# Kernel tuning notes

Hardware: AMD Instinct MI355X
Metric: run time of the kernel (lower is better)

## Reference

```python
import jax, jax.numpy as jnp
import numpy as np

B, S, H = 8, 512, 1024          # batch, seq_len, hidden_size
T, K, FF = 8, 2, 4096           # num_thoughts, top_k, ffn dim (4*H)
NH = 8                          # combiner attention heads
HD = H // NH
CREATIVITY = 1.0


def setup_inputs() -> dict:
    key = jax.random.key(0)
    ks = jax.random.split(key, 16)
    s = 0.02
    return {
        "hidden_states": jax.random.normal(ks[0], (B, S, H), jnp.float32),
        # router
        "router_w": jax.random.normal(ks[1], (H, T), jnp.float32) * s,
        "router_b": jnp.zeros((T,), jnp.float32),
        # thought branch FFNs (one per thought)
        "W1": jax.random.normal(ks[2], (T, H, FF), jnp.float32) * s,
        "b1": jnp.zeros((T, FF), jnp.float32),
        "W2": jax.random.normal(ks[3], (T, FF, H), jnp.float32) * s,
        "b2": jnp.zeros((T, H), jnp.float32),
        # attention combiner (MultiheadAttention proj weights)
        "Wq": jax.random.normal(ks[4], (H, H), jnp.float32) * s,
        "bq": jnp.zeros((H,), jnp.float32),
        "Wk": jax.random.normal(ks[5], (H, H), jnp.float32) * s,
        "bk": jnp.zeros((H,), jnp.float32),
        "Wv": jax.random.normal(ks[6], (H, H), jnp.float32) * s,
        "bv": jnp.zeros((H,), jnp.float32),
        "Wo": jax.random.normal(ks[7], (H, H), jnp.float32) * s,
        "bo": jnp.zeros((H,), jnp.float32),
    }


def reference(hidden_states, router_w, router_b, W1, b1, W2, b2,
              Wq, bq, Wk, bk, Wv, bv, Wo, bo):
    # ---- router: mean-pool -> linear -> softmax -> top-k ----
    pooled = hidden_states.mean(axis=1)                       # [B,H]
    router_probs = jax.nn.softmax(pooled @ router_w + router_b, axis=-1)  # [B,T]
    top_p, top_i = jax.lax.top_k(router_probs, K)             # [B,K]
    weights = jax.nn.softmax(top_p, axis=-1)                  # renormalized active weights [B,K]

    # ---- grouped branch FFN (gather expert weights, batched GEMMs) ----
    h = jnp.einsum('bsh,bkhf->bksf', hidden_states, W1[top_i]) + b1[top_i][:, :, None, :]
    h = jax.nn.gelu(h, approximate=False)
    branch_out = jnp.einsum('bksf,bkfh->bksh', h, W2[top_i]) + b2[top_i][:, :, None, :]
    branch_out = branch_out * CREATIVITY                      # [B,K,S,H]

    # ---- attention combiner over flattened thoughts [B, K*S, H] ----
    L = K * S
    flat = branch_out.reshape(B, L, H)
    q = (flat @ Wq + bq).reshape(B, L, NH, HD)
    k = (flat @ Wk + bk).reshape(B, L, NH, HD)
    v = (flat @ Wv + bv).reshape(B, L, NH, HD)
    scores = jnp.einsum('blhd,bmhd->bhlm', q, k) / jnp.sqrt(jnp.float32(HD))
    attn = jax.nn.softmax(scores, axis=-1)
    ctx = jnp.einsum('bhlm,bmhd->blhd', attn, v).reshape(B, L, H)
    attended = (ctx @ Wo + bo).reshape(B, K, S, H)

    combined = jnp.einsum('bksh,bk->bsh', attended, weights)  # [B,S,H]

    # ---- metrics ----
    entropy = jnp.mean(-jnp.sum(router_probs * jnp.log(router_probs + 1e-8), axis=1))
    a = branch_out[:, 0].reshape(B, -1)
    b_ = branch_out[:, 1].reshape(B, -1)
    cos = jnp.sum(a * b_, -1) / jnp.maximum(
        jnp.linalg.norm(a, axis=-1) * jnp.linalg.norm(b_, axis=-1), 1e-8)
    diversity = jnp.mean(1.0 - cos)
    return combined, entropy, diversity
```

## Files before the change

### kernel.cpp

```cpp
#include <hip/hip_runtime.h>
#include <hip/hip_bf16.h>
#include <math.h>

typedef float f32x4 __attribute__((ext_vector_type(4)));
typedef short s16x8 __attribute__((ext_vector_type(8)));
typedef short s16x4 __attribute__((ext_vector_type(4)));
typedef unsigned int u32;

#define DEVI __device__ __forceinline__

#define Bn   8
#define Sn   512
#define Hn   1024
#define Tn   8
#define Kn   2
#define FFn  4096
#define NHn  8
#define HDn  128
#define Ln   1024
#define OUT_COMBINED 4194304

DEVI unsigned short f2bf(float x) {
  __hip_bfloat16 h = __float2bfloat16(x);
  union { __hip_bfloat16 h; unsigned short u; } cv; cv.h = h; return cv.u;
}
DEVI float bf2f(unsigned short u) {
  union { u32 i; float f; } cv; cv.i = ((u32)u) << 16; return cv.f;
}
DEVI float gelu_f(float x) {
  float t = x * x * x;
  float y = 0.7978845608028654f * x + 0.03567740813f * t;
  float e = exp2f(2.8853900817779268f * y);
  return x - x / (e + 1.0f);
}

typedef __attribute__((address_space(3))) u32 lds_u32;
typedef __attribute__((address_space(1))) u32 glb_u32;
DEVI void gload16(const void* g, void* l) {
  __builtin_amdgcn_global_load_lds((const glb_u32*)g, (lds_u32*)l, 16, 0, 0);
}

__global__ __launch_bounds__(256) void pool_part_k(const float* __restrict__ hid, float* __restrict__ part)
{
  const int b = blockIdx.x, scn = blockIdx.y;
  const int hh = threadIdx.x * 4;
  float4 acc = make_float4(0.f, 0.f, 0.f, 0.f);
  const float* base = hid + ((long)b * Sn + (long)scn * 128) * Hn + hh;
  for (int s = 0; s < 128; ++s) {
    float4 v = *(const float4*)(base + (long)s * Hn);
    acc.x += v.x; acc.y += v.y; acc.z += v.z; acc.w += v.w;
  }
  *(float4*)(part + ((long)(scn * Bn + b)) * Hn + hh) = acc;
}

__global__ __launch_bounds__(256) void pool_final_k(const float* __restrict__ part, float* __restrict__ pooled)
{
  const int i = blockIdx.x * 256 + threadIdx.x;
  float s = 0.f;
  for (int sc = 0; sc < 4; ++sc) s += part[sc * (Bn * Hn) + i];
  pooled[i] = s * (1.f / (float)Sn);
}

__global__ __launch_bounds__(256) void router_k(
    const float* __restrict__ pooled, const float* __restrict__ rw, const float* __restrict__ rb,
    float* __restrict__ probs, int* __restrict__ topi, float* __restrict__ wts,
    int* __restrict__ flags, float* __restrict__ entropy_out)
{
  __shared__ float partial[256];
  __shared__ float lg[64];
  __shared__ int sfl[8];
  __shared__ float sent[8];
  const int tid = threadIdx.x;
  const int bt = tid & 63, slice = tid >> 6;
  const int b = bt >> 3, t = bt & 7;
  if (tid < 8) sfl[tid] = 0;
  float acc = 0.f;
  const float* pb = pooled + b * Hn;
  for (int i = slice * 256; i < slice * 256 + 256; ++i) acc += pb[i] * rw[i * Tn + t];
  partial[tid] = acc;
  __syncthreads();
  if (tid < 64) lg[tid] = rb[t] + partial[tid] + partial[tid + 64] + partial[tid + 128] + partial[tid + 192];
  __syncthreads();
  if (tid < 64 && t == 0) {
    float p[8];
    float mx = lg[b * 8];
    for (int i = 1; i < 8; ++i) mx = fmaxf(mx, lg[b * 8 + i]);
    float ssum = 0.f;
    for (int i = 0; i < 8; ++i) { p[i] = expf(lg[b * 8 + i] - mx); ssum += p[i]; }
    float ent = 0.f;
    for (int i = 0; i < 8; ++i) { p[i] /= ssum; ent -= p[i] * logf(p[i] + 1e-8f); probs[b * 8 + i] = p[i]; }
    sent[b] = ent;
    int i1 = 0;
    for (int i = 1; i < 8; ++i) if (p[i] > p[i1]) i1 = i;
    int i2 = (i1 == 0) ? 1 : 0;
    for (int i = 0; i < 8; ++i) if (i != i1 && p[i] > p[i2]) i2 = i;
    float w0 = 1.f / (1.f + expf(p[i2] - p[i1]));
    float w1 = 1.f / (1.f + expf(p[i1] - p[i2]));
    topi[b * 2] = i1; topi[b * 2 + 1] = i2;
    wts[b * 2] = w0; wts[b * 2 + 1] = w1;
    atomicOr(&sfl[i1], 1); atomicOr(&sfl[i2], 1);
  }
  __syncthreads();
  if (tid < 8) flags[tid] = sfl[tid];
  if (tid == 0) {
    float e = 0.f;
    for (int i = 0; i < 8; ++i) e += sent[i];
    entropy_out[0] = e * (1.f / (float)Bn);
  }
}

__global__ __launch_bounds__(256) void cvt_k(const float* __restrict__ in, unsigned short* __restrict__ out)
{
  const long i = ((long)blockIdx.x * 256 + threadIdx.x) * 4;
  float4 v = *(const float4*)(in + i);
  s16x4 o;
  o[0] = (short)f2bf(v.x); o[1] = (short)f2bf(v.y); o[2] = (short)f2bf(v.z); o[3] = (short)f2bf(v.w);
  *(s16x4*)(out + i) = o;
}

__global__ __launch_bounds__(256) void bias3_k(const float* __restrict__ bq, const float* __restrict__ bk,
                                               const float* __restrict__ bv, float* __restrict__ o)
{
  const int i = blockIdx.x * 256 + threadIdx.x;
  o[i] = bq[i]; o[i + 1024] = bk[i]; o[i + 2048] = bv[i];
}

__global__ __launch_bounds__(256) void transpose_k(const float* __restrict__ Win, unsigned short* __restrict__ Wout,
                                                   int Kd, int N, long sIn, long sOut, const int* __restrict__ flags)
{
  const int t = blockIdx.z;
  if (flags && flags[t] == 0) return;
  __shared__ float tile[64][65];
  const float* in = Win + (long)t * sIn;
  unsigned short* out = Wout + (long)t * sOut;
  const int kb = blockIdx.y * 64, nb = blockIdx.x * 64;
  const int tx = threadIdx.x & 15, ty = threadIdx.x >> 4;
  #pragma unroll
  for (int i = 0; i < 4; ++i) {
    const int r = ty + i * 16;
    float4 v = *(const float4*)(in + (long)(kb + r) * N + nb + tx * 4);
    tile[r][tx * 4 + 0] = v.x; tile[r][tx * 4 + 1] = v.y;
    tile[r][tx * 4 + 2] = v.z; tile[r][tx * 4 + 3] = v.w;
  }
  __syncthreads();
  #pragma unroll
  for (int i = 0; i < 4; ++i) {
    const int n = ty + i * 16;
    s16x4 o;
    #pragma unroll
    for (int j = 0; j < 4; ++j) o[j] = (short)f2bf(tile[tx * 4 + j][n]);
    *(s16x4*)(out + (long)(nb + n) * Kd + kb + tx * 4) = o;
  }
}

template<int EPI, int OUTMODE>
__global__ __launch_bounds__(256, 2) void gemmT_k(
    const unsigned short* __restrict__ A0, const unsigned short* __restrict__ Bt0,
    const float* __restrict__ bias0, unsigned short* __restrict__ C0,
    int N, int Kd,
    const int* __restrict__ topi, int kTop,
    long sA_b, long sA_p, long sBt_t, int sBias_t, long sC_p)
{
  __shared__ __align__(16) char smem[73728];
  char* const Ab = smem;
  char* const Bb = smem + 49152;

  const int gx = gridDim.x, gy = gridDim.y;
  const int nwg = gx * gy * gridDim.z;
  const int hw = blockIdx.x + gx * (blockIdx.y + gy * blockIdx.z);
  const int q = nwg >> 3, r = nwg & 7;
  const int xcd = hw & 7, sub = hw >> 3;
  int lin = (xcd < r ? xcd * (q + 1) : r * (q + 1) + (xcd - r) * q) + sub;
  const int bx = lin % gx; lin /= gx;
  const int by = lin % gy;
  const int bz = lin / gy;

  const int bidx = kTop ? (bz / kTop) : 0;
  const int te = topi ? topi[bz] : 0;
  const unsigned short* A = A0 + (long)bidx * sA_b + (long)bz * sA_p;
  const unsigned short* Bt = Bt0 + (long)te * sBt_t;
  const float* bias = bias0 + (long)te * sBias_t;
  unsigned short* C = C0 + (long)bz * sC_p;

  const int m0 = by * 256;
  const int n0 = bx * 128;
  const int tid = threadIdx.x;
  const int lane = tid & 63, w = tid >> 6;
  const int wm = w >> 1, wn = w & 1;
  const int rA = lane & 15, g = lane >> 4;

  const int sr = lane >> 2;
  const int sc = lane & 3;
  const int csw = (sc ^ ((sr >> 1) & 3)) * 8;
  const unsigned short* gAw = A + (long)(m0 + w * 64 + sr) * Kd + csw;
  const unsigned short* gBw = Bt + (long)(n0 + w * 32 + sr) * Kd + csw;
  const int ldso = lane << 4;

  const int sl = (rA >> 1) & 3;
  int aoff[8], boff[4];
  #pragma unroll
  for (int mi = 0; mi < 8; ++mi)
    aoff[mi] = (wm * 128 + mi * 16 + rA) * 64 + ((g ^ sl) << 4);
  #pragma unroll
  for (int nj = 0; nj < 4; ++nj)
    boff[nj] = (wn * 64 + nj * 16 + rA) * 64 + ((g ^ sl) << 4);

  f32x4 acc[8][4];
  const f32x4 zero = {0.f, 0.f, 0.f, 0.f};
  #pragma unroll
  for (int i = 0; i < 8; ++i)
    #pragma unroll
    for (int j = 0; j < 4; ++j) acc[i][j] = zero;

  const int nt = Kd >> 5;

  auto stageA = [&](int kt2, int buf, int i) {
    gload16(gAw + (long)i * 16 * Kd + kt2 * 32, Ab + buf * 16384 + w * 4096 + i * 1024 + ldso);
  };
  auto stageB = [&](int kt2, int buf, int i) {
    gload16(gBw + (long)i * 16 * Kd + kt2 * 32, Bb + buf * 8192 + w * 2048 + i * 1024 + ldso);
  };

  #pragma unroll
  for (int j = 0; j < 2; ++j) {
    stageA(j, j, 0); stageA(j, j, 1); stageB(j, j, 0);
    stageA(j, j, 2); stageA(j, j, 3); stageB(j, j, 1);
  }
  asm volatile("s_waitcnt vmcnt(6)" ::: "memory");
  __builtin_amdgcn_s_barrier();

  int cb = 0, fb = 2;
  for (int kt = 0; kt < nt; ++kt) {
    const char* pa = Ab + cb * 16384;
    const char* pb = Bb + cb * 8192;
    const bool st = (kt + 2 < nt);
    const int ft = kt + 2;

    s16x8 af[8], bf[4];
    #pragma unroll
    for (int mi = 0; mi < 4; ++mi) af[mi] = *(const s16x8*)(pa + aoff[mi]);
    #pragma unroll
    for (int nj = 0; nj < 4; ++nj) bf[nj] = *(const s16x8*)(pb + boff[nj]);
    if (st) { stageA(ft, fb, 0); stageA(ft, fb, 1); stageB(ft, fb, 0); }
    #pragma unroll
    for (int mi = 0; mi < 4; ++mi) af[4 + mi] = *(const s16x8*)(pa + aoff[4 + mi]);
    if (st) { stageA(ft, fb, 2); stageA(ft, fb, 3); stageB(ft, fb, 1); }

    __builtin_amdgcn_s_setprio(1);
    #pragma unroll
    for (int mi = 0; mi < 8; ++mi)
      #pragma unroll
      for (int nj = 0; nj < 4; ++nj)
        acc[mi][nj] = __builtin_amdgcn_mfma_f32_16x16x32_bf16(af[mi], bf[nj], acc[mi][nj], 0, 0, 0);
    __builtin_amdgcn_s_setprio(0);

    if (st)                asm volatile("s_waitcnt vmcnt(6) lgkmcnt(0)" ::: "memory");
    else if (kt + 1 < nt)  asm volatile("s_waitcnt vmcnt(0) lgkmcnt(0)" ::: "memory");
    else                   asm volatile("s_waitcnt lgkmcnt(0)" ::: "memory");
    __builtin_amdgcn_s_barrier();
    cb = (cb + 1 == 3) ? 0 : cb + 1;
    fb = (fb + 1 == 3) ? 0 : fb + 1;
  }

  __syncthreads();

  unsigned short* et = (unsigned short*)(smem + w * 9216);
  const int r4 = g << 2;
  const int nbase = n0 + wn * 64;
  const int seg = (OUTMODE == 1) ? (nbase >> 10) : 0;
  const int erow = lane >> 3, echunk = lane & 7;
  float bv[4];
  #pragma unroll
  for (int nj = 0; nj < 4; ++nj) bv[nj] = bias[nbase + nj * 16 + rA];

  #pragma unroll
  for (int p = 0; p < 2; ++p) {
    #pragma unroll
    for (int nj = 0; nj < 4; ++nj) {
      #pragma unroll
      for (int mi2 = 0; mi2 < 4; ++mi2) {
        #pragma unroll
        for (int j = 0; j < 4; ++j) {
          float x = acc[p * 4 + mi2][nj][j] + bv[nj];
          if (EPI == 1) x = gelu_f(x);
          const int mrl = mi2 * 16 + r4 + j;
          const int ncl = nj * 16 + rA;
          if (OUTMODE == 0 || seg < 2) et[mrl * 72 + ncl] = f2bf(x);
          else                         et[ncl * 72 + mrl] = f2bf(x);
        }
      }
    }
    const long mrow0 = m0 + wm * 128 + p * 64;
    if (OUTMODE == 0) {
      #pragma unroll
      for (int rr = 0; rr < 8; ++rr) {
        const int row = rr * 8 + erow;
        s16x8 v = *(const s16x8*)(et + row * 72 + echunk * 8);
        *(s16x8*)(C + (mrow0 + row) * N + nbase + echunk * 8) = v;
      }
    } else {
      const int nseg = nbase & 1023;
      if (seg < 2) {
        unsigned short* dst = C + (long)seg * 8388608;
        #pragma unroll
        for (int rr = 0; rr < 8; ++rr) {
          const int row = rr * 8 + erow;
          s16x8 v = *(const s16x8*)(et + row * 72 + echunk * 8);
          *(s16x8*)(dst + (mrow0 + row) * 1024 + nseg + echunk * 8) = v;
        }
      } else {
        unsigned short* vtp = C + 16777216;
        const int bb = (int)(mrow0 >> 10);
        const int ltok0 = (int)(mrow0 & 1023);
        #pragma unroll
        for (int rr = 0; rr < 8; ++rr) {
          const int nrow = rr * 8 + erow;
          s16x8 v = *(const s16x8*)(et + nrow * 72 + echunk * 8);
          *(s16x8*)(vtp + ((long)(bb * 1024 + nseg + nrow)) * 1024 + ltok0 + echunk * 8) = v;
        }
      }
    }
  }
}

__global__ __launch_bounds__(256) void flash_k(
    const unsigned short* __restrict__ q, const unsigned short* __restrict__ k,
    const unsigned short* __restrict__ vt, unsigned short* __restrict__ ctx)
{
  __shared__ unsigned short K2[2][64 * 128];
  __shared__ unsigned short Vs[128 * 64];
  __shared__ unsigned short Ps[4][32 * 72];
  const int L = blockIdx.x;
  const int qt = L >> 6;
  const int hb = (((L >> 3) & 7) << 3) + (L & 7);
  const int h = hb & 7, b = hb >> 3;
  const int tid = threadIdx.x, lane = tid & 63, w = tid >> 6;
  const int rA = lane & 15, g = lane >> 4;
  const int q0w = qt * 128 + w * 32;

  s16x8 qf[2][4];
  #pragma unroll
  for (int qi = 0; qi < 2; ++qi) {
    const unsigned short* qp = q + ((long)(b * Ln + q0w + qi * 16 + rA)) * Hn + h * HDn + g * 8;
    #pragma unroll
    for (int kk = 0; kk < 4; ++kk) qf[qi][kk] = *(const s16x8*)(qp + kk * 32);
  }
  asm volatile("s_waitcnt vmcnt(0)" ::: "memory");

  f32x4 o[2][8];
  const f32x4 zero = {0.f, 0.f, 0.f, 0.f};
  #pragma unroll
  for (int qi = 0; qi < 2; ++qi)
    #pragma unroll
    for (int nn = 0; nn < 8; ++nn) o[qi][nn] = zero;
  float lrun[2][4];
  #pragma unroll
  for (int qi = 0; qi < 2; ++qi)
    #pragma unroll
    for (int j = 0; j < 4; ++j) lrun[qi][j] = 0.f;
  float m = 0.f;

  const float sc2 = 0.08838834764831845f * 1.4426950408889634f;

  const int krow0 = w * 16 + g;
  const int kc = lane & 15;
  const int vrow0 = w * 32 + (lane >> 3);
  const int vc = lane & 7;

  auto issueK = [&](int kvt2, int buf) {
    const int kv0 = kvt2 * 64;
    #pragma unroll
    for (int qq = 0; qq < 4; ++qq) {
      const int rk = krow0 + qq * 4;
      gload16(k + ((long)(b * Ln + kv0 + rk)) * Hn + h * HDn + ((kc ^ (rk & 7)) * 8),
              (char*)K2[buf] + w * 4096 + qq * 1024);
    }
  };
  auto issueV = [&](int kvt2) {
    const int kv0 = kvt2 * 64;
    #pragma unroll
    for (int qq = 0; qq < 4; ++qq) {
      const int rv = vrow0 + qq * 8;
      gload16(vt + ((long)(b * 1024 + h * HDn + rv)) * Ln + kv0 + ((vc ^ (rv & 7)) * 8),
              (char*)Vs + w * 4096 + qq * 1024);
    }
  };

  issueK(0, 0);
  asm volatile("s_waitcnt vmcnt(0)" ::: "memory");
  __builtin_amdgcn_s_barrier();

  for (int kvt = 0; kvt < 16; ++kvt) {
    const bool st = (kvt + 1 < 16);
    const char* Kcur = (const char*)K2[kvt & 1];
    issueV(kvt);
    if (st) issueK(kvt + 1, (kvt + 1) & 1);

    f32x4 sacc[2][4];
    #pragma unroll
    for (int qi = 0; qi < 2; ++qi)
      #pragma unroll
      for (int nj = 0; nj < 4; ++nj) sacc[qi][nj] = zero;
    __builtin_amdgcn_s_setprio(1);
    #pragma unroll
    for (int kk = 0; kk < 4; ++kk) {
      #pragma unroll
      for (int nj = 0; nj < 4; ++nj) {
        const int row = nj * 16 + rA;
        const int byt = row * 256 + (((kk * 4 + g) ^ (row & 7)) << 4);
        s16x8 kf = *(const s16x8*)(Kcur + byt);
        sacc[0][nj] = __builtin_amdgcn_mfma_f32_16x16x32_bf16(qf[0][kk], kf, sacc[0][nj], 0, 0, 0);
        sacc[1][nj] = __builtin_amdgcn_mfma_f32_16x16x32_bf16(qf[1][kk], kf, sacc[1][nj], 0, 0, 0);
      }
    }
    __builtin_amdgcn_s_setprio(0);

    float vmax = -3.0e38f;
    #pragma unroll
    for (int qi = 0; qi < 2; ++qi)
      #pragma unroll
      for (int nj = 0; nj < 4; ++nj)
        #pragma unroll
        for (int j = 0; j < 4; ++j) {
          const float s = sacc[qi][nj][j] * sc2;
          sacc[qi][nj][j] = s;
          vmax = fmaxf(vmax, s);
        }
    if (!__all(vmax <= m + 8.0f)) {
      float mn = vmax;
      #pragma unroll
      for (int mm = 1; mm < 64; mm <<= 1) mn = fmaxf(mn, __shfl_xor(mn, mm, 64));
      const float al = exp2f(m - mn);
      #pragma unroll
      for (int qi = 0; qi < 2; ++qi) {
        #pragma unroll
        for (int nn = 0; nn < 8; ++nn)
          #pragma unroll
          for (int j = 0; j < 4; ++j) o[qi][nn][j] *= al;
        #pragma unroll
        for (int j = 0; j < 4; ++j) lrun[qi][j] *= al;
      }
      m = mn;
    }

    if (st) asm volatile("s_waitcnt vmcnt(4)" ::: "memory");
    else    asm volatile("s_waitcnt vmcnt(0)" ::: "memory");
    __builtin_amdgcn_s_barrier();

    #pragma unroll
    for (int qi = 0; qi < 2; ++qi)
      #pragma unroll
      for (int j = 0; j < 4; ++j) {
        float p0 = exp2f(sacc[qi][0][j] - m);
        float p1 = exp2f(sacc[qi][1][j] - m);
        float p2 = exp2f(sacc[qi][2][j] - m);
        float p3 = exp2f(sacc[qi][3][j] - m);
        lrun[qi][j] += (p0 + p1) + (p2 + p3);
        const int prow = (qi * 16 + g * 4 + j) * 72;
        Ps[w][prow + 0 * 16 + rA] = f2bf(p0);
        Ps[w][prow + 1 * 16 + rA] = f2bf(p1);
        Ps[w][prow + 2 * 16 + rA] = f2bf(p2);
        Ps[w][prow + 3 * 16 + rA] = f2bf(p3);
      }

    s16x8 pf[2][2];
    #pragma unroll
    for (int qi = 0; qi < 2; ++qi)
      #pragma unroll
      for (int kk2 = 0; kk2 < 2; ++kk2)
        pf[qi][kk2] = *(const s16x8*)(&Ps[w][(qi * 16 + rA) * 72 + kk2 * 32 + g * 8]);
    __builtin_amdgcn_s_setprio(1);
    #pragma unroll
    for (int kk2 = 0; kk2 < 2; ++kk2) {
      #pragma unroll
      for (int nn = 0; nn < 8; ++nn) {
        const int row = nn * 16 + rA;
        const int byt = row * 128 + (((kk2 * 4 + g) ^ (row & 7)) << 4);
        s16x8 vf = *(const s16x8*)((const char*)Vs + byt);
        o[0][nn] = __builtin_amdgcn_mfma_f32_16x16x32_bf16(pf[0][kk2], vf, o[0][nn], 0, 0, 0);
        o[1][nn] = __builtin_amdgcn_mfma_f32_16x16x32_bf16(pf[1][kk2], vf, o[1][nn], 0, 0, 0);
      }
    }
    __builtin_amdgcn_s_setprio(0);

    if (st) asm volatile("s_waitcnt vmcnt(0) lgkmcnt(0)" ::: "memory");
    else    asm volatile("s_waitcnt lgkmcnt(0)" ::: "memory");
    __builtin_amdgcn_s_barrier();
  }

  float linv[2][4];
  #pragma unroll
  for (int qi = 0; qi < 2; ++qi)
    #pragma unroll
    for (int j = 0; j < 4; ++j) {
      float l = lrun[qi][j];
      #pragma unroll
      for (int mm = 1; mm < 16; mm <<= 1) l += __shfl_xor(l, mm, 64);
      linv[qi][j] = 1.0f / l;
    }
  #pragma unroll
  for (int qi = 0; qi < 2; ++qi)
    #pragma unroll
    for (int nn = 0; nn < 8; ++nn)
      #pragma unroll
      for (int j = 0; j < 4; ++j) {
        const int row = q0w + qi * 16 + g * 4 + j;
        ctx[((long)(b * Ln + row)) * Hn + h * HDn + nn * 16 + rA] = f2bf(o[qi][nn][j] * linv[qi][j]);
      }
}

__global__ __launch_bounds__(256) void div_part_k(const unsigned short* __restrict__ br, float* __restrict__ part)
{
  const int b = blockIdx.y, ch = blockIdx.x;
  const unsigned short* a = br + (long)b * (2L * Sn * Hn);
  const unsigned short* c = a + (long)Sn * Hn;
  const int base = ch * 16384 + threadIdx.x * 8;
  float dot = 0.f, na = 0.f, nb = 0.f;
  #pragma unroll
  for (int i = 0; i < 8; ++i) {
    const int idx = base + i * 2048;
    s16x8 av = *(const s16x8*)(a + idx);
    s16x8 cv = *(const s16x8*)(c + idx);
    #pragma unroll
    for (int e = 0; e < 8; ++e) {
      float fa = bf2f((unsigned short)av[e]);
      float fc = bf2f((unsigned short)cv[e]);
      dot += fa * fc; na += fa * fa; nb += fc * fc;
    }
  }
  #pragma unroll
  for (int mm = 1; mm < 64; mm <<= 1) {
    dot += __shfl_xor(dot, mm, 64);
    na  += __shfl_xor(na, mm, 64);
    nb  += __shfl_xor(nb, mm, 64);
  }
  __shared__ float red[12];
  const int lane = threadIdx.x & 63, w = threadIdx.x >> 6;
  if (lane == 0) { red[w * 3] = dot; red[w * 3 + 1] = na; red[w * 3 + 2] = nb; }
  __syncthreads();
  if (threadIdx.x == 0) {
    float d = 0, x = 0, y = 0;
    for (int i = 0; i < 4; ++i) { d += red[i * 3]; x += red[i * 3 + 1]; y += red[i * 3 + 2]; }
    float* op = part + ((long)(b * 32 + ch)) * 3;
    op[0] = d; op[1] = x; op[2] = y;
  }
}

__global__ __launch_bounds__(64) void div_final_k(const float* __restrict__ part, float* __restrict__ outp)
{
  __shared__ float cosr[8];
  const int tid = threadIdx.x;
  if (tid < 8) {
    float d = 0, x = 0, y = 0;
    for (int i = 0; i < 32; ++i) {
      const float* p = part + ((long)(tid * 32 + i)) * 3;
      d += p[0]; x += p[1]; y += p[2];
    }
    cosr[tid] = d / fmaxf(sqrtf(x) * sqrtf(y), 1e-8f);
  }
  __syncthreads();
  if (tid == 0) {
    float s = 0.f;
    for (int i = 0; i < 8; ++i) s += 1.f - cosr[i];
    outp[0] = s * (1.f / 8.f);
  }
}

__global__ __launch_bounds__(256) void combine_k(const unsigned short* __restrict__ att,
                                                 const float* __restrict__ wts, float* __restrict__ out)
{
  const long i = ((long)blockIdx.x * 256 + threadIdx.x) * 8;
  const int b = (int)(i >> 19);
  const long rem = i & 524287;
  const unsigned short* a0 = att + (long)b * (2L * Sn * Hn) + rem;
  const unsigned short* a1 = a0 + (long)Sn * Hn;
  const float w0 = wts[b * 2], w1 = wts[b * 2 + 1];
  s16x8 v0 = *(const s16x8*)a0;
  s16x8 v1 = *(const s16x8*)a1;
  float r[8];
  #pragma unroll
  for (int e = 0; e < 8; ++e) r[e] = w0 * bf2f((unsigned short)v0[e]) + w1 * bf2f((unsigned short)v1[e]);
  *(float4*)(out + i)     = make_float4(r[0], r[1], r[2], r[3]);
  *(float4*)(out + i + 4) = make_float4(r[4], r[5], r[6], r[7]);
}

extern "C" void kernel_launch(void* const* d_in, const int* in_sizes, int n_in,
                              void* d_out, int out_size, void* d_ws, size_t ws_size,
                              hipStream_t stream)
{
  (void)in_sizes; (void)n_in; (void)out_size; (void)ws_size;
  const float* hidden   = (const float*)d_in[0];
  const float* router_w = (const float*)d_in[1];
  const float* router_b = (const float*)d_in[2];
  const float* W1 = (const float*)d_in[3];
  const float* b1 = (const float*)d_in[4];
  const float* W2 = (const float*)d_in[5];
  const float* b2 = (const float*)d_in[6];
  const float* Wq = (const float*)d_in[7];
  const float* bq = (const float*)d_in[8];
  const float* Wk = (const float*)d_in[9];
  const float* bk = (const float*)d_in[10];
  const float* Wv = (const float*)d_in[11];
  const float* bv = (const float*)d_in[12];
  const float* Wo = (const float*)d_in[13];
  const float* bo = (const float*)d_in[14];
  float* out = (float*)d_out;

  char* ws = (char*)d_ws;
  float* pooled  = (float*)(ws);
  float* ppart   = (float*)(ws + 32768);
  float* probs   = (float*)(ws + 163840);
  int*   topi    = (int*)  (ws + 164096);
  float* wts     = (float*)(ws + 164352);
  int*   flags   = (int*)  (ws + 164608);
  float* dpart   = (float*)(ws + 164864);
  float* qkvbias = (float*)(ws + 167936);
  unsigned short* hid_bf = (unsigned short*)(ws + 262144);
  unsigned short* Wt     = (unsigned short*)(ws + 262144 + 8388608);
  unsigned short* hbuf   = (unsigned short*)(ws + 262144 + 8388608 + 67108864);
  unsigned short* br     = (unsigned short*)(ws + 262144 + 8388608 + 134217728);
  unsigned short* wqkvo  = (unsigned short*)(ws + 262144 + 8388608 + 134217728 + 16777216);
  unsigned short* qb  = Wt;
  unsigned short* kbf = Wt + 8388608;
  unsigned short* vt  = Wt + 16777216;
  unsigned short* ctx = hbuf;
  unsigned short* att = hbuf + 8388608;
  unsigned short* wqt = wqkvo;
  unsigned short* wkt = wqkvo + 1048576;
  unsigned short* wvt = wqkvo + 2097152;
  unsigned short* wot = wqkvo + 3145728;

  pool_part_k<<<dim3(Bn, 4), 256, 0, stream>>>(hidden, ppart);
  pool_final_k<<<dim3(32), 256, 0, stream>>>(ppart, pooled);
  router_k<<<1, 256, 0, stream>>>(pooled, router_w, router_b, probs, topi, wts, flags, out + OUT_COMBINED);

  cvt_k<<<4096, 256, 0, stream>>>(hidden, hid_bf);
  bias3_k<<<4, 256, 0, stream>>>(bq, bk, bv, qkvbias);
  transpose_k<<<dim3(64, 16, Tn), 256, 0, stream>>>(W1, Wt, Hn, FFn, (long)Hn * FFn, (long)FFn * Hn, flags);
  transpose_k<<<dim3(16, 16, 1), 256, 0, stream>>>(Wq, wqt, Hn, Hn, 0, 0, nullptr);
  transpose_k<<<dim3(16, 16, 1), 256, 0, stream>>>(Wk, wkt, Hn, Hn, 0, 0, nullptr);
  transpose_k<<<dim3(16, 16, 1), 256, 0, stream>>>(Wv, wvt, Hn, Hn, 0, 0, nullptr);
  transpose_k<<<dim3(16, 16, 1), 256, 0, stream>>>(Wo, wot, Hn, Hn, 0, 0, nullptr);

  gemmT_k<1, 0><<<dim3(FFn / 128, Sn / 256, 16), 256, 0, stream>>>(
      hid_bf, Wt, b1, hbuf, FFn, Hn, topi, 2,
      (long)Sn * Hn, 0L, (long)FFn * Hn, FFn, (long)Sn * FFn);

  transpose_k<<<dim3(16, 64, Tn), 256, 0, stream>>>(W2, Wt, FFn, Hn, (long)FFn * Hn, (long)Hn * FFn, flags);

  gemmT_k<0, 0><<<dim3(Hn / 128, Sn / 256, 16), 256, 0, stream>>>(
      hbuf, Wt, b2, br, Hn, FFn, topi, 2,
      0L, (long)Sn * FFn, (long)Hn * FFn, Hn, (long)Sn * Hn);

  div_part_k<<<dim3(32, Bn), 256, 0, stream>>>(br, dpart);
  div_final_k<<<1, 64, 0, stream>>>(dpart, out + OUT_COMBINED + 1);

  gemmT_k<0, 1><<<dim3(3072 / 128, (Bn * Ln) / 256, 1), 256, 0, stream>>>(
      br, wqkvo, qkvbias, qb, 3072, Hn, nullptr, 0, 0L, 0L, 0L, 0, 0L);

  flash_k<<<dim3(512), 256, 0, stream>>>(qb, kbf, vt, ctx);

  gemmT_k<0, 0><<<dim3(Hn / 128, (Bn * Ln) / 256, 1), 256, 0, stream>>>(
      ctx, wot, bo, att, Hn, Hn, nullptr, 0, 0L, 0L, 0L, 0, 0L);

  combine_k<<<2048, 256, 0, stream>>>(att, wts, out);
}
```

Baseline: 517.1 us.

## Pool from bf16 hidden copy and defer attention wait past softmax

Runs the bf16 conversion before pooling so the pooling kernel reads half the bytes. This changes router numerics slightly, because the mean is now taken over bf16-rounded values. In the attention kernel, K/V global pointers are precomputed and advanced incrementally instead of being recomputed each tile. The row-max reduction becomes a tree, and the vmcnt wait plus barrier move after the exp/P-store so V loads overlap more of the softmax work.

Result: no change. 509.2 us (-1.5%).

```diff
diff --git a/kernel.cpp b/kernel.cpp
--- a/kernel.cpp
+++ b/kernel.cpp
@@ -40,15 +40,16 @@
   __builtin_amdgcn_global_load_lds((const glb_u32*)g, (lds_u32*)l, 16, 0, 0);
 }
 
-__global__ __launch_bounds__(256) void pool_part_k(const float* __restrict__ hid, float* __restrict__ part)
+__global__ __launch_bounds__(256) void pool_part_k(const unsigned short* __restrict__ hid, float* __restrict__ part)
 {
   const int b = blockIdx.x, scn = blockIdx.y;
   const int hh = threadIdx.x * 4;
   float4 acc = make_float4(0.f, 0.f, 0.f, 0.f);
-  const float* base = hid + ((long)b * Sn + (long)scn * 128) * Hn + hh;
+  const unsigned short* base = hid + ((long)b * Sn + (long)scn * 128) * Hn + hh;
   for (int s = 0; s < 128; ++s) {
-    float4 v = *(const float4*)(base + (long)s * Hn);
-    acc.x += v.x; acc.y += v.y; acc.z += v.z; acc.w += v.w;
+    s16x4 v = *(const s16x4*)(base + (long)s * Hn);
+    acc.x += bf2f((unsigned short)v[0]); acc.y += bf2f((unsigned short)v[1]);
+    acc.z += bf2f((unsigned short)v[2]); acc.w += bf2f((unsigned short)v[3]);
   }
   *(float4*)(part + ((long)(scn * Bn + b)) * Hn + hh) = acc;
 }
@@ -367,34 +368,40 @@
   const int vrow0 = w * 32 + (lane >> 3);
   const int vc = lane & 7;
 
-  auto issueK = [&](int kvt2, int buf) {
-    const int kv0 = kvt2 * 64;
+  const unsigned short* kp[4];
+  const unsigned short* vp[4];
+  #pragma unroll
+  for (int qq = 0; qq < 4; ++qq) {
+    const int rk = krow0 + qq * 4;
+    kp[qq] = k + ((long)(b * Ln + rk)) * Hn + h * HDn + ((kc ^ (rk & 7)) * 8);
+    const int rv = vrow0 + qq * 8;
+    vp[qq] = vt + ((long)(b * 1024 + h * HDn + rv)) * Ln + ((vc ^ (rv & 7)) * 8);
+  }
+
+  auto issueK = [&](int buf) {
     #pragma unroll
     for (int qq = 0; qq < 4; ++qq) {
-      const int rk = krow0 + qq * 4;
-      gload16(k + ((long)(b * Ln + kv0 + rk)) * Hn + h * HDn + ((kc ^ (rk & 7)) * 8),
-              (char*)K2[buf] + w * 4096 + qq * 1024);
+      gload16(kp[qq], (char*)K2[buf] + w * 4096 + qq * 1024);
+      kp[qq] += 64 * Hn;
     }
   };
-  auto issueV = [&](int kvt2) {
-    const int kv0 = kvt2 * 64;
+  auto issueV = [&]() {
     #pragma unroll
     for (int qq = 0; qq < 4; ++qq) {
-      const int rv = vrow0 + qq * 8;
-      gload16(vt + ((long)(b * 1024 + h * HDn + rv)) * Ln + kv0 + ((vc ^ (rv & 7)) * 8),
-              (char*)Vs + w * 4096 + qq * 1024);
+      gload16(vp[qq], (char*)Vs + w * 4096 + qq * 1024);
+      vp[qq] += 64;
     }
   };
 
-  issueK(0, 0);
+  issueK(0);
   asm volatile("s_waitcnt vmcnt(0)" ::: "memory");
   __builtin_amdgcn_s_barrier();
 
   for (int kvt = 0; kvt < 16; ++kvt) {
     const bool st = (kvt + 1 < 16);
     const char* Kcur = (const char*)K2[kvt & 1];
-    issueV(kvt);
-    if (st) issueK(kvt + 1, (kvt + 1) & 1);
+    issueV();
+    if (st) issueK((kvt + 1) & 1);
 
     f32x4 sacc[2][4];
     #pragma unroll
@@ -415,17 +422,21 @@
     }
     __builtin_amdgcn_s_setprio(0);
 
-    float vmax = -3.0e38f;
+    float t8[8];
     #pragma unroll
     for (int qi = 0; qi < 2; ++qi)
       #pragma unroll
-      for (int nj = 0; nj < 4; ++nj)
-        #pragma unroll
-        for (int j = 0; j < 4; ++j) {
-          const float s = sacc[qi][nj][j] * sc2;
-          sacc[qi][nj][j] = s;
-          vmax = fmaxf(vmax, s);
-        }
+      for (int nj = 0; nj < 4; ++nj) {
+        float s0 = sacc[qi][nj][0] * sc2;
+        float s1 = sacc[qi][nj][1] * sc2;
+        float s2 = sacc[qi][nj][2] * sc2;
+        float s3 = sacc[qi][nj][3] * sc2;
+        sacc[qi][nj][0] = s0; sacc[qi][nj][1] = s1;
+        sacc[qi][nj][2] = s2; sacc[qi][nj][3] = s3;
+        t8[qi * 4 + nj] = fmaxf(fmaxf(s0, s1), fmaxf(s2, s3));
+      }
+    const float vmax = fmaxf(fmaxf(fmaxf(t8[0], t8[1]), fmaxf(t8[2], t8[3])),
+                             fmaxf(fmaxf(t8[4], t8[5]), fmaxf(t8[6], t8[7])));
     if (!__all(vmax <= m + 8.0f)) {
       float mn = vmax;
       #pragma unroll
@@ -442,10 +453,6 @@
       }
       m = mn;
     }
-
-    if (st) asm volatile("s_waitcnt vmcnt(4)" ::: "memory");
-    else    asm volatile("s_waitcnt vmcnt(0)" ::: "memory");
-    __builtin_amdgcn_s_barrier();
 
     #pragma unroll
     for (int qi = 0; qi < 2; ++qi)
@@ -462,6 +469,10 @@
         Ps[w][prow + 2 * 16 + rA] = f2bf(p2);
         Ps[w][prow + 3 * 16 + rA] = f2bf(p3);
       }
+
+    if (st) asm volatile("s_waitcnt vmcnt(4)" ::: "memory");
+    else    asm volatile("s_waitcnt vmcnt(0)" ::: "memory");
+    __builtin_amdgcn_s_barrier();
 
     s16x8 pf[2][2];
     #pragma unroll
@@ -630,11 +641,12 @@
   unsigned short* wvt = wqkvo + 2097152;
   unsigned short* wot = wqkvo + 3145728;
 
-  pool_part_k<<<dim3(Bn, 4), 256, 0, stream>>>(hidden, ppart);
+  cvt_k<<<4096, 256, 0, stream>>>(hidden, hid_bf);
+
+  pool_part_k<<<dim3(Bn, 4), 256, 0, stream>>>(hid_bf, ppart);
   pool_final_k<<<dim3(32), 256, 0, stream>>>(ppart, pooled);
   router_k<<<1, 256, 0, stream>>>(pooled, router_w, router_b, probs, topi, wts, flags, out + OUT_COMBINED);
 
-  cvt_k<<<4096, 256, 0, stream>>>(hidden, hid_bf);
   bias3_k<<<4, 256, 0, stream>>>(bq, bk, bv, qkvbias);
   transpose_k<<<dim3(64, 16, Tn), 256, 0, stream>>>(W1, Wt, Hn, FFn, (long)Hn * FFn, (long)FFn * Hn, flags);
   transpose_k<<<dim3(16, 16, 1), 256, 0, stream>>>(Wq, wqt, Hn, Hn, 0, 0, nullptr);
```
